# Performance work log

Measured on AMD Instinct MI355X. Metric: run time of the kernel, lower is better.

Reference implementation:

```python
import jax, jax.numpy as jnp
import numpy as np

NUM_HEADS = 8


def setup_inputs() -> dict:
    key = jax.random.key(0)
    ks = jax.random.split(key, 8)
    b, m, d = 8, 2048, 512
    sc = 1.0 / np.sqrt(d)
    return {
        "x": jax.random.normal(ks[0], (b, m, d), jnp.float32),
        "w_q": jax.random.normal(ks[1], (d, d), jnp.float32) * sc,
        "w_k": jax.random.normal(ks[2], (d, d), jnp.float32) * sc,
        "w_v": jax.random.normal(ks[3], (d, d), jnp.float32) * sc,
        "in_proj_w": jax.random.normal(ks[4], (3 * d, d), jnp.float32) * sc,
        "in_proj_b": jax.random.normal(ks[5], (3 * d,), jnp.float32) * 0.01,
        "out_w": jax.random.normal(ks[6], (d, d), jnp.float32) * sc,
        "out_b": jax.random.normal(ks[7], (d,), jnp.float32) * 0.01,
    }


def _rope_cos_sin(m, d):
    # faithful to source: theta = 10000 ** (-2*(i-1)/d), i = 0..d/2-1
    i = jnp.arange(d // 2, dtype=jnp.float32)
    theta = jnp.power(10000.0, -2.0 * (i - 1.0) / d)
    ang = jnp.arange(m, dtype=jnp.float32)[:, None] * theta  # [m, d/2]
    return jnp.cos(ang), jnp.sin(ang)


def reference(x, w_q, w_k, w_v, in_proj_w, in_proj_b, out_w, out_b):
    b, m, d = x.shape
    h, hd = NUM_HEADS, d // NUM_HEADS
    c, s = _rope_cos_sin(m, d)

    def rot(t):
        # equivalent to t[pos] @ R[pos] with the source's block-rotation matrix
        te = t.reshape(b, m, d // 2, 2)
        e, o = te[..., 0], te[..., 1]
        return jnp.stack([e * c + o * s, -e * s + o * c], axis=-1).reshape(b, m, d)

    q = rot(x @ w_q.T)
    k = rot(x @ w_k.T)
    v = rot(x @ w_v.T)

    # nn.MultiheadAttention's internal in_proj
    wqi, wki, wvi = jnp.split(in_proj_w, 3, axis=0)
    bqi, bki, bvi = jnp.split(in_proj_b, 3, axis=0)
    q = (q @ wqi.T + bqi).reshape(b, m, h, hd)
    k = (k @ wki.T + bki).reshape(b, m, h, hd)
    v = (v @ wvi.T + bvi).reshape(b, m, h, hd)

    scale = 1.0 / jnp.sqrt(jnp.asarray(hd, x.dtype))
    scores = jnp.einsum("bqhd,bkhd->bhqk", q, k) * scale
    causal = jnp.triu(jnp.ones((m, m), bool), k=1)
    scores = jnp.where(causal, jnp.finfo(x.dtype).min, scores)
    attn = jax.nn.softmax(scores, axis=-1)
    ctx = jnp.einsum("bhqk,bkhd->bqhd", attn, v).reshape(b, m, d)
    return ctx @ out_w.T + out_b
```

## Files before the change

### kernel.cpp

```cpp
#include <hip/hip_runtime.h>
#include <hip/hip_bf16.h>

typedef __attribute__((ext_vector_type(8))) short short8;
typedef __attribute__((ext_vector_type(4))) short short4v;
typedef __attribute__((ext_vector_type(4))) float f32x4;

__device__ __forceinline__ float bf2f(unsigned short u) {
    union { unsigned int i; float f; } v; v.i = ((unsigned int)u) << 16; return v.f;
}
__device__ __forceinline__ unsigned short f2bfh(float f) {
    union { __hip_bfloat16 h; unsigned short u; } c;
    c.h = __float2bfloat16(f);
    return c.u;
}

#define GLDS16(g, l) __builtin_amdgcn_global_load_lds( \
    (const __attribute__((address_space(1))) unsigned int*)(g), \
    (__attribute__((address_space(3))) unsigned int*)(l), 16, 0, 0)

__global__ __launch_bounds__(256) void cvt_one(
    const float* __restrict__ in, unsigned short* __restrict__ out, int nchunk)
{
    int i = blockIdx.x * 256 + threadIdx.x;
    if (i >= nchunk) return;
    f32x4 a = *(const f32x4*)&in[(size_t)i * 8];
    f32x4 b = *(const f32x4*)&in[(size_t)i * 8 + 4];
    short8 o;
    o[0] = (short)f2bfh(a[0]); o[1] = (short)f2bfh(a[1]);
    o[2] = (short)f2bfh(a[2]); o[3] = (short)f2bfh(a[3]);
    o[4] = (short)f2bfh(b[0]); o[5] = (short)f2bfh(b[1]);
    o[6] = (short)f2bfh(b[2]); o[7] = (short)f2bfh(b[3]);
    *(short8*)&out[(size_t)i * 8] = o;
}

__global__ __launch_bounds__(256) void cvt_w(
    const float* __restrict__ wq, const float* __restrict__ wk, const float* __restrict__ wv,
    const float* __restrict__ ipw, const float* __restrict__ ow,
    unsigned short* __restrict__ wqb, unsigned short* __restrict__ ipwb,
    unsigned short* __restrict__ owb)
{
    int z = blockIdx.y;
    const float* src;
    unsigned short* dst;
    if (z < 3)      { src = (z == 0 ? wq : z == 1 ? wk : wv); dst = wqb + (size_t)z * 262144; }
    else if (z < 6) { src = ipw + (size_t)(z - 3) * 262144;   dst = ipwb + (size_t)(z - 3) * 262144; }
    else            { src = ow;                                dst = owb; }
    int i = blockIdx.x * 256 + threadIdx.x;
    f32x4 a = *(const f32x4*)&src[(size_t)i * 8];
    f32x4 b = *(const f32x4*)&src[(size_t)i * 8 + 4];
    short8 o;
    o[0] = (short)f2bfh(a[0]); o[1] = (short)f2bfh(a[1]);
    o[2] = (short)f2bfh(a[2]); o[3] = (short)f2bfh(a[3]);
    o[4] = (short)f2bfh(b[0]); o[5] = (short)f2bfh(b[1]);
    o[6] = (short)f2bfh(b[2]); o[7] = (short)f2bfh(b[3]);
    *(short8*)&dst[(size_t)i * 8] = o;
}

__global__ __launch_bounds__(256) void rope_table(float* __restrict__ ct, float* __restrict__ st)
{
    int i = blockIdx.x;
    const float THC = -0.05190512648261308f;
    float theta = exp2f(THC * ((float)i - 1.0f));
    for (int k = 0; k < 8; ++k) {
        int pos = k * 256 + threadIdx.x;
        float sn, cs;
        sincosf((float)pos * theta, &sn, &cs);
        ct[i * 2048 + pos] = cs;
        st[i * 2048 + pos] = sn;
    }
}

__device__ __forceinline__ void gemm_core(
    const unsigned short* __restrict__ A, int lda,
    const unsigned short* __restrict__ B, int K,
    int rowBase, int colBase, int tid, int lane, int wave,
    short* As, short* Bs, f32x4 (&acc)[4][4])
{
    const int wr = wave >> 1, wc = wave & 1;
    const int lo = lane & 15, hi = lane >> 4;
    for (int k0 = 0; k0 < K; k0 += 64) {
        const unsigned short* Ab = A + (size_t)rowBase * lda + k0;
        const unsigned short* Bb = B + (size_t)colBase * K + k0;
        #pragma unroll
        for (int p = 0; p < 4; ++p) {
            int o = p * 256 + tid;
            GLDS16(&Ab[(size_t)(o >> 3) * lda + (o & 7) * 8], &As[o * 8]);
        }
        #pragma unroll
        for (int p = 0; p < 4; ++p) {
            int o = p * 256 + tid;
            GLDS16(&Bb[(size_t)(o >> 3) * K + (o & 7) * 8], &Bs[o * 8]);
        }
        __syncthreads();
        #pragma unroll
        for (int s = 0; s < 2; ++s) {
            short8 a[4], b[4];
            #pragma unroll
            for (int i = 0; i < 4; ++i)
                a[i] = *(const short8*)&As[(wr * 64 + i * 16 + lo) * 64 + s * 32 + hi * 8];
            #pragma unroll
            for (int j = 0; j < 4; ++j)
                b[j] = *(const short8*)&Bs[(wc * 64 + j * 16 + lo) * 64 + s * 32 + hi * 8];
            #pragma unroll
            for (int i = 0; i < 4; ++i)
                #pragma unroll
                for (int j = 0; j < 4; ++j)
                    acc[i][j] = __builtin_amdgcn_mfma_f32_16x16x32_bf16(a[i], b[j], acc[i][j], 0, 0, 0);
        }
        __syncthreads();
    }
}

template<int HAS_BIAS, int OUT>
__global__ __launch_bounds__(256) void gemm_bt(
    const unsigned short* __restrict__ A, int lda, const unsigned short* __restrict__ B,
    const float* __restrict__ bias, void* __restrict__ Cp,
    int M, int N, int K)
{
    __shared__ __align__(16) short As[128 * 64];
    __shared__ __align__(16) short Bs[128 * 64];
    const int tid = threadIdx.x, lane = tid & 63, wave = tid >> 6;
    const int wr = wave >> 1, wc = wave & 1;
    const int lo = lane & 15, hi = lane >> 4;
    const int rowBase = blockIdx.y * 128;
    const int colBase = blockIdx.x * 128;

    f32x4 acc[4][4] = {};
    gemm_core(A, lda, B, K, rowBase, colBase, tid, lane, wave, As, Bs, acc);

    #pragma unroll
    for (int i = 0; i < 4; ++i) {
        int rowA = rowBase + wr * 64 + i * 16 + hi * 4;
        #pragma unroll
        for (int j = 0; j < 4; ++j) {
            int col = colBase + wc * 64 + j * 16 + lo;
            float bv = HAS_BIAS ? bias[col] : 0.0f;
            #pragma unroll
            for (int r = 0; r < 4; ++r) {
                float v = acc[i][j][r] + bv;
                if (OUT == 1) ((float*)Cp)[(size_t)(rowA + r) * N + col] = v;
                else          ((unsigned short*)Cp)[(size_t)(rowA + r) * N + col] = f2bfh(v);
            }
        }
    }
}

__global__ __launch_bounds__(256) void gemm_rope(
    const unsigned short* __restrict__ A, const unsigned short* __restrict__ B,
    unsigned short* __restrict__ T,
    const float* __restrict__ ct, const float* __restrict__ st)
{
    __shared__ __align__(16) short As[128 * 64];
    __shared__ __align__(16) short Bs[128 * 64];
    const int tid = threadIdx.x, lane = tid & 63, wave = tid >> 6;
    const int wr = wave >> 1, wc = wave & 1;
    const int lo = lane & 15, hi = lane >> 4;
    const int rowBase = blockIdx.y * 128;
    const int colBase = blockIdx.x * 128;

    f32x4 acc[4][4] = {};
    gemm_core(A, 512, B, 512, rowBase, colBase, tid, lane, wave, As, Bs, acc);

    const float sgn = (lane & 1) ? -1.0f : 1.0f;
    #pragma unroll
    for (int i = 0; i < 4; ++i) {
        int rowA = rowBase + wr * 64 + i * 16 + hi * 4;
        int pos0 = rowA & 2047;
        #pragma unroll
        for (int j = 0; j < 4; ++j) {
            int col = colBase + wc * 64 + j * 16 + lo;
            int ii = (col & 511) >> 1;
            f32x4 cs = *(const f32x4*)&ct[ii * 2048 + pos0];
            f32x4 sn = *(const f32x4*)&st[ii * 2048 + pos0];
            #pragma unroll
            for (int r = 0; r < 4; ++r) {
                float v = acc[i][j][r];
                float p = __shfl_xor(v, 1);
                float o = v * cs[r] + sgn * p * sn[r];
                T[(size_t)(rowA + r) * 1536 + col] = f2bfh(o);
            }
        }
    }
}

__global__ __launch_bounds__(256) void gemm_inproj(
    const unsigned short* __restrict__ T, const unsigned short* __restrict__ ipwb,
    const float* __restrict__ ipb,
    unsigned short* __restrict__ Qb, unsigned short* __restrict__ Kb,
    unsigned short* __restrict__ Vt)
{
    __shared__ __align__(16) short As[128 * 64];
    __shared__ __align__(16) short Bs[128 * 64];
    const int tid = threadIdx.x, lane = tid & 63, wave = tid >> 6;
    const int wr = wave >> 1, wc = wave & 1;
    const int lo = lane & 15, hi = lane >> 4;
    const int rowBase = blockIdx.y * 128;
    const int colBase = blockIdx.x * 128;
    const int z = blockIdx.z;

    const unsigned short* A = T + z * 512;
    const unsigned short* B = ipwb + (size_t)z * 262144;
    const float* bias = ipb + z * 512;

    f32x4 acc[4][4] = {};
    gemm_core(A, 1536, B, 512, rowBase, colBase, tid, lane, wave, As, Bs, acc);

    unsigned short* Crm = (z == 0) ? Qb : Kb;
    #pragma unroll
    for (int i = 0; i < 4; ++i) {
        int rowA = rowBase + wr * 64 + i * 16 + hi * 4;
        #pragma unroll
        for (int j = 0; j < 4; ++j) {
            int col = colBase + wc * 64 + j * 16 + lo;
            float bv = bias[col];
            if (z == 2) {
                short4v sv;
                #pragma unroll
                for (int r = 0; r < 4; ++r) sv[r] = (short)f2bfh(acc[i][j][r] + bv);
                size_t idx = (((size_t)(rowA >> 11) * 8 + (col >> 6)) * 64 + (col & 63)) * 2048
                             + (rowA & 2047);
                *(short4v*)&Vt[idx] = sv;
            } else {
                #pragma unroll
                for (int r = 0; r < 4; ++r)
                    Crm[(size_t)(rowA + r) * 512 + col] = f2bfh(acc[i][j][r] + bv);
            }
        }
    }
}


__device__ __forceinline__ void attn_step(
    int kt, int NT, int qrow, int lo, int hi,
    const short* __restrict__ KsB, const short* __restrict__ VsB,
    short* __restrict__ Pw,
    short8 (&aq)[2], f32x4 (&o_acc)[4],
    float (&m_i)[4], float (&l_i)[4])
{
    const int swz = (lo & 7) << 3;

    f32x4 sa[4] = {};
    #pragma unroll
    for (int s = 0; s < 2; ++s) {
        short8 bk[4];
        #pragma unroll
        for (int n = 0; n < 4; ++n)
            bk[n] = *(const short8*)&KsB[(n * 16 + lo) * 64 + ((s * 32 + hi * 8) ^ swz)];
        #pragma unroll
        for (int n = 0; n < 4; ++n)
            sa[n] = __builtin_amdgcn_mfma_f32_16x16x32_bf16(aq[s], bk[n], sa[n], 0, 0, 0);
    }

    const bool need_mask = (kt == NT - 1);
    float sv[4][4];
    #pragma unroll
    for (int n = 0; n < 4; ++n) {
        int key = kt * 64 + n * 16 + lo;
        #pragma unroll
        for (int r = 0; r < 4; ++r) {
            float x = sa[n][r];
            if (need_mask) {
                int qr = qrow + hi * 4 + r;
                if (key > qr) x = -1e30f;
            }
            sv[n][r] = x;
        }
    }

    float alpha[4];
    #pragma unroll
    for (int r = 0; r < 4; ++r) {
        float x = fmaxf(fmaxf(sv[0][r], sv[1][r]), fmaxf(sv[2][r], sv[3][r]));
        #pragma unroll
        for (int off = 1; off < 16; off <<= 1) x = fmaxf(x, __shfl_xor(x, off));
        float mn = fmaxf(m_i[r], x);
        alpha[r] = __expf(m_i[r] - mn);
        m_i[r] = mn;
    }
    #pragma unroll
    for (int n = 0; n < 4; ++n)
        #pragma unroll
        for (int r = 0; r < 4; ++r)
            sv[n][r] = __expf(sv[n][r] - m_i[r]);

    #pragma unroll
    for (int r = 0; r < 4; ++r)
        l_i[r] = l_i[r] * alpha[r] + (sv[0][r] + sv[1][r]) + (sv[2][r] + sv[3][r]);

    #pragma unroll
    for (int t = 0; t < 4; ++t)
        #pragma unroll
        for (int r = 0; r < 4; ++r)
            o_acc[t][r] *= alpha[r];

    #pragma unroll
    for (int n = 0; n < 4; ++n)
        #pragma unroll
        for (int r = 0; r < 4; ++r) {
            int prow = hi * 4 + r;
            Pw[prow * 64 + ((n * 16 + lo) ^ ((prow & 7) << 3))] = (short)f2bfh(sv[n][r]);
        }

    #pragma unroll
    for (int s = 0; s < 2; ++s) {
        short8 ap = *(const short8*)&Pw[lo * 64 + ((s * 32 + hi * 8) ^ swz)];
        #pragma unroll
        for (int t = 0; t < 4; ++t) {
            short8 bv = *(const short8*)&VsB[(t * 16 + lo) * 64 + ((s * 32 + hi * 8) ^ swz)];
            o_acc[t] = __builtin_amdgcn_mfma_f32_16x16x32_bf16(ap, bv, o_acc[t], 0, 0, 0);
        }
    }
}

#define STG_LOAD(kt, KR0, KR1, VR0, VR1) { \
    int rr = tid >> 3, cc = (tid & 7) * 8; \
    KR0 = *(const short8*)&Kp[(rowQ + (size_t)((kt) * 64 + rr)) * 512 + colBase + cc]; \
    KR1 = *(const short8*)&Kp[(rowQ + (size_t)((kt) * 64 + rr + 32)) * 512 + colBase + cc]; \
    VR0 = *(const short8*)&Vh[(size_t)rr * 2048 + (kt) * 64 + cc]; \
    VR1 = *(const short8*)&Vh[(size_t)(rr + 32) * 2048 + (kt) * 64 + cc]; }

#define STG_WRITE(BUF, KR0, KR1, VR0, VR1) { \
    int rr = tid >> 3; \
    int sw = ((tid & 7) * 8) ^ ((rr & 7) << 3); \
    *(short8*)&Ks[BUF][rr * 64 + sw] = KR0; \
    *(short8*)&Ks[BUF][(rr + 32) * 64 + sw] = KR1; \
    *(short8*)&Vs[BUF][rr * 64 + sw] = VR0; \
    *(short8*)&Vs[BUF][(rr + 32) * 64 + sw] = VR1; }

__global__ __launch_bounds__(256, 3) void attn_kernel(
    const unsigned short* __restrict__ Q, const unsigned short* __restrict__ Kp,
    const unsigned short* __restrict__ Vt, unsigned short* __restrict__ O)
{
    const int tid = threadIdx.x, lane = tid & 63, wave = tid >> 6;
    const int lo = lane & 15, hi = lane >> 4;
    const int bh = blockIdx.x;
    const int qb = 31 - blockIdx.y;
    const int bb = bh >> 3, hh = bh & 7;
    const int NT = qb + 1;

    __shared__ __align__(16) short Ks[2][64 * 64];
    __shared__ __align__(16) short Vs[2][64 * 64];
    __shared__ __align__(16) short P[4][16 * 64];
    short* Pw = P[wave];

    const size_t rowQ = (size_t)bb * 2048;
    const int colBase = hh * 64;
    const unsigned short* Vh = Vt + (size_t)bh * 64 * 2048;
    const int qrow = qb * 64 + wave * 16;

    short8 aq[2];
    #pragma unroll
    for (int s = 0; s < 2; ++s) {
        aq[s] = *(const short8*)&Q[(rowQ + qrow + lo) * 512 + colBase + s * 32 + hi * 8];
        #pragma unroll
        for (int e = 0; e < 8; ++e)
            aq[s][e] = (short)f2bfh(bf2f((unsigned short)aq[s][e]) * 0.125f);
    }

    f32x4 o_acc[4] = {};
    float m_i[4], l_i[4];
    #pragma unroll
    for (int r = 0; r < 4; ++r) { m_i[r] = -1e30f; l_i[r] = 0.0f; }

    short8 ka0, ka1, va0, va1;
    short8 kb0, kb1, vb0, vb1;

    STG_LOAD(0, ka0, ka1, va0, va1);
    STG_WRITE(0, ka0, ka1, va0, va1);
    if (1 < NT) STG_LOAD(1, kb0, kb1, vb0, vb1);
    __syncthreads();

    for (int kt = 0; kt < NT; ) {
        if (kt + 1 < NT) STG_WRITE(1, kb0, kb1, vb0, vb1);
        if (kt + 2 < NT) STG_LOAD(kt + 2, ka0, ka1, va0, va1);
        attn_step(kt, NT, qrow, lo, hi, Ks[0], Vs[0], Pw, aq, o_acc, m_i, l_i);
        __syncthreads();
        ++kt;
        if (kt >= NT) break;
        if (kt + 1 < NT) STG_WRITE(0, ka0, ka1, va0, va1);
        if (kt + 2 < NT) STG_LOAD(kt + 2, kb0, kb1, vb0, vb1);
        attn_step(kt, NT, qrow, lo, hi, Ks[1], Vs[1], Pw, aq, o_acc, m_i, l_i);
        __syncthreads();
        ++kt;
    }

    #pragma unroll
    for (int r = 0; r < 4; ++r) {
        float x = l_i[r];
        #pragma unroll
        for (int off = 1; off < 16; off <<= 1) x += __shfl_xor(x, off);
        l_i[r] = x;
    }

    #pragma unroll
    for (int t = 0; t < 4; ++t)
        #pragma unroll
        for (int r = 0; r < 4; ++r) {
            float v = o_acc[t][r] / l_i[r];
            O[(rowQ + qrow + hi * 4 + r) * 512 + colBase + t * 16 + lo] = f2bfh(v);
        }
}

extern "C" void kernel_launch(void* const* d_in, const int* in_sizes, int n_in,
                              void* d_out, int out_size, void* d_ws, size_t ws_size,
                              hipStream_t stream)
{
    (void)in_sizes; (void)n_in; (void)out_size; (void)ws_size;
    const float* x   = (const float*)d_in[0];
    const float* w_q = (const float*)d_in[1];
    const float* w_k = (const float*)d_in[2];
    const float* w_v = (const float*)d_in[3];
    const float* ipw = (const float*)d_in[4];
    const float* ipb = (const float*)d_in[5];
    const float* ow  = (const float*)d_in[6];
    const float* ob  = (const float*)d_in[7];

    const int M = 16384;
    const size_t SZ = (size_t)M * 512;
    unsigned short* xb   = (unsigned short*)d_ws;
    unsigned short* wqb  = xb + SZ;
    unsigned short* ipwb = wqb + 786432;
    unsigned short* owb  = ipwb + 786432;
    unsigned short* T    = owb + 262144;
    unsigned short* Kb   = T + (size_t)M * 1536;
    unsigned short* Vt   = Kb + SZ;
    float* ct = (float*)(Vt + SZ);
    float* st = ct + 524288;
    unsigned short* Qb   = xb;
    unsigned short* Cb   = T;

    dim3 blk(256);

    cvt_one<<<dim3((int)(SZ / 8 / 256)), blk, 0, stream>>>(x, xb, (int)(SZ / 8));
    cvt_w<<<dim3(128, 7), blk, 0, stream>>>(w_q, w_k, w_v, ipw, ow, wqb, ipwb, owb);
    rope_table<<<dim3(256), blk, 0, stream>>>(ct, st);

    gemm_rope<<<dim3(12, 128), blk, 0, stream>>>(xb, wqb, T, ct, st);

    gemm_inproj<<<dim3(4, 128, 3), blk, 0, stream>>>(T, ipwb, ipb, Qb, Kb, Vt);

    attn_kernel<<<dim3(64, 32), blk, 0, stream>>>(Qb, Kb, Vt, Cb);

    gemm_bt<1, 1><<<dim3(4, 128), blk, 0, stream>>>(Cb, 512, owb, ob, (float*)d_out, M, 512, 512);
}
```

Before: 316.0 us.

## Compute transposed scores so P feeds PV MFMA from registers, dropping LDS round-trip

Swaps the operands of the QK^T MFMA so each lane holds a column of keys for one query row. The softmax row max and sum then need only two cross-lane shuffles instead of four. The probabilities are packed straight into 16x16x16 bf16 MFMA A-operands, which removes the per-wave P scratch in shared memory, its stores and reloads. The cost is twice as many, smaller PV MFMAs, extra shuffles to broadcast alpha and l to the output layout, and narrower V reads from LDS.

```diff
diff --git a/kernel.cpp b/kernel.cpp
--- a/kernel.cpp
+++ b/kernel.cpp
@@ -17,6 +17,12 @@
 #define GLDS16(g, l) __builtin_amdgcn_global_load_lds( \
     (const __attribute__((address_space(1))) unsigned int*)(g), \
     (__attribute__((address_space(3))) unsigned int*)(l), 16, 0, 0)
+
+#if __has_builtin(__builtin_amdgcn_mfma_f32_16x16x16_bf16)
+#define MFMA_PV(a, b, c) __builtin_amdgcn_mfma_f32_16x16x16_bf16(a, b, c, 0, 0, 0)
+#else
+#define MFMA_PV(a, b, c) __builtin_amdgcn_mfma_f32_16x16x16bf16_1k(a, b, c, 0, 0, 0)
+#endif
 
 __global__ __launch_bounds__(256) void cvt_one(
     const float* __restrict__ in, unsigned short* __restrict__ out, int nchunk)
@@ -233,9 +239,8 @@
 __device__ __forceinline__ void attn_step(
     int kt, int NT, int qrow, int lo, int hi,
     const short* __restrict__ KsB, const short* __restrict__ VsB,
-    short* __restrict__ Pw,
     short8 (&aq)[2], f32x4 (&o_acc)[4],
-    float (&m_i)[4], float (&l_i)[4])
+    float &m_i, float &l_i)
 {
     const int swz = (lo & 7) << 3;
 
@@ -248,68 +253,71 @@
             bk[n] = *(const short8*)&KsB[(n * 16 + lo) * 64 + ((s * 32 + hi * 8) ^ swz)];
         #pragma unroll
         for (int n = 0; n < 4; ++n)
-            sa[n] = __builtin_amdgcn_mfma_f32_16x16x32_bf16(aq[s], bk[n], sa[n], 0, 0, 0);
+            sa[n] = __builtin_amdgcn_mfma_f32_16x16x32_bf16(bk[n], aq[s], sa[n], 0, 0, 0);
     }
 
     const bool need_mask = (kt == NT - 1);
+    const int q = qrow + lo;
     float sv[4][4];
     #pragma unroll
-    for (int n = 0; n < 4; ++n) {
-        int key = kt * 64 + n * 16 + lo;
+    for (int n = 0; n < 4; ++n)
         #pragma unroll
         for (int r = 0; r < 4; ++r) {
             float x = sa[n][r];
             if (need_mask) {
-                int qr = qrow + hi * 4 + r;
-                if (key > qr) x = -1e30f;
+                int key = kt * 64 + n * 16 + hi * 4 + r;
+                if (key > q) x = -1e30f;
             }
             sv[n][r] = x;
         }
-    }
-
-    float alpha[4];
-    #pragma unroll
-    for (int r = 0; r < 4; ++r) {
-        float x = fmaxf(fmaxf(sv[0][r], sv[1][r]), fmaxf(sv[2][r], sv[3][r]));
-        #pragma unroll
-        for (int off = 1; off < 16; off <<= 1) x = fmaxf(x, __shfl_xor(x, off));
-        float mn = fmaxf(m_i[r], x);
-        alpha[r] = __expf(m_i[r] - mn);
-        m_i[r] = mn;
-    }
+
+    float mx0 = fmaxf(fmaxf(sv[0][0], sv[0][1]), fmaxf(sv[0][2], sv[0][3]));
+    float mx1 = fmaxf(fmaxf(sv[1][0], sv[1][1]), fmaxf(sv[1][2], sv[1][3]));
+    float mx2 = fmaxf(fmaxf(sv[2][0], sv[2][1]), fmaxf(sv[2][2], sv[2][3]));
+    float mx3 = fmaxf(fmaxf(sv[3][0], sv[3][1]), fmaxf(sv[3][2], sv[3][3]));
+    float mx = fmaxf(fmaxf(mx0, mx1), fmaxf(mx2, mx3));
+    mx = fmaxf(mx, __shfl_xor(mx, 16));
+    mx = fmaxf(mx, __shfl_xor(mx, 32));
+    float mn = fmaxf(m_i, mx);
+    float alpha = __expf(m_i - mn);
+    m_i = mn;
+
     #pragma unroll
     for (int n = 0; n < 4; ++n)
         #pragma unroll
         for (int r = 0; r < 4; ++r)
-            sv[n][r] = __expf(sv[n][r] - m_i[r]);
-
+            sv[n][r] = __expf(sv[n][r] - mn);
+
+    float s0 = (sv[0][0] + sv[0][1]) + (sv[0][2] + sv[0][3]);
+    float s1 = (sv[1][0] + sv[1][1]) + (sv[1][2] + sv[1][3]);
+    float s2 = (sv[2][0] + sv[2][1]) + (sv[2][2] + sv[2][3]);
+    float s3 = (sv[3][0] + sv[3][1]) + (sv[3][2] + sv[3][3]);
+    l_i = l_i * alpha + ((s0 + s1) + (s2 + s3));
+
+    float ar[4];
     #pragma unroll
     for (int r = 0; r < 4; ++r)
-        l_i[r] = l_i[r] * alpha[r] + (sv[0][r] + sv[1][r]) + (sv[2][r] + sv[3][r]);
-
+        ar[r] = __shfl(alpha, hi * 4 + r);
     #pragma unroll
     for (int t = 0; t < 4; ++t)
         #pragma unroll
         for (int r = 0; r < 4; ++r)
-            o_acc[t][r] *= alpha[r];
-
+            o_acc[t][r] *= ar[r];
+
+    short4v pa[4];
     #pragma unroll
     for (int n = 0; n < 4; ++n)
         #pragma unroll
-        for (int r = 0; r < 4; ++r) {
-            int prow = hi * 4 + r;
-            Pw[prow * 64 + ((n * 16 + lo) ^ ((prow & 7) << 3))] = (short)f2bfh(sv[n][r]);
-        }
-
-    #pragma unroll
-    for (int s = 0; s < 2; ++s) {
-        short8 ap = *(const short8*)&Pw[lo * 64 + ((s * 32 + hi * 8) ^ swz)];
+        for (int r = 0; r < 4; ++r)
+            pa[n][r] = (short)f2bfh(sv[n][r]);
+
+    #pragma unroll
+    for (int n = 0; n < 4; ++n)
         #pragma unroll
         for (int t = 0; t < 4; ++t) {
-            short8 bv = *(const short8*)&VsB[(t * 16 + lo) * 64 + ((s * 32 + hi * 8) ^ swz)];
-            o_acc[t] = __builtin_amdgcn_mfma_f32_16x16x32_bf16(ap, bv, o_acc[t], 0, 0, 0);
-        }
-    }
+            short4v vb = *(const short4v*)&VsB[(t * 16 + lo) * 64 + ((n * 16 + hi * 4) ^ swz)];
+            o_acc[t] = MFMA_PV(pa[n], vb, o_acc[t]);
+        }
 }
 
 #define STG_LOAD(kt, KR0, KR1, VR0, VR1) { \
@@ -340,8 +348,6 @@
 
     __shared__ __align__(16) short Ks[2][64 * 64];
     __shared__ __align__(16) short Vs[2][64 * 64];
-    __shared__ __align__(16) short P[4][16 * 64];
-    short* Pw = P[wave];
 
     const size_t rowQ = (size_t)bb * 2048;
     const int colBase = hh * 64;
@@ -358,9 +364,7 @@
     }
 
     f32x4 o_acc[4] = {};
-    float m_i[4], l_i[4];
-    #pragma unroll
-    for (int r = 0; r < 4; ++r) { m_i[r] = -1e30f; l_i[r] = 0.0f; }
+    float m_i = -1e30f, l_i = 0.0f;
 
     short8 ka0, ka1, va0, va1;
     short8 kb0, kb1, vb0, vb1;
@@ -373,30 +377,30 @@
     for (int kt = 0; kt < NT; ) {
         if (kt + 1 < NT) STG_WRITE(1, kb0, kb1, vb0, vb1);
         if (kt + 2 < NT) STG_LOAD(kt + 2, ka0, ka1, va0, va1);
-        attn_step(kt, NT, qrow, lo, hi, Ks[0], Vs[0], Pw, aq, o_acc, m_i, l_i);
+        attn_step(kt, NT, qrow, lo, hi, Ks[0], Vs[0], aq, o_acc, m_i, l_i);
         __syncthreads();
         ++kt;
         if (kt >= NT) break;
         if (kt + 1 < NT) STG_WRITE(0, ka0, ka1, va0, va1);
         if (kt + 2 < NT) STG_LOAD(kt + 2, kb0, kb1, vb0, vb1);
-        attn_step(kt, NT, qrow, lo, hi, Ks[1], Vs[1], Pw, aq, o_acc, m_i, l_i);
+        attn_step(kt, NT, qrow, lo, hi, Ks[1], Vs[1], aq, o_acc, m_i, l_i);
         __syncthreads();
         ++kt;
     }
 
-    #pragma unroll
-    for (int r = 0; r < 4; ++r) {
-        float x = l_i[r];
-        #pragma unroll
-        for (int off = 1; off < 16; off <<= 1) x += __shfl_xor(x, off);
-        l_i[r] = x;
-    }
+    float lt = l_i;
+    lt += __shfl_xor(lt, 16);
+    lt += __shfl_xor(lt, 32);
+    float lr[4];
+    #pragma unroll
+    for (int r = 0; r < 4; ++r)
+        lr[r] = __shfl(lt, hi * 4 + r);
 
     #pragma unroll
     for (int t = 0; t < 4; ++t)
         #pragma unroll
         for (int r = 0; r < 4; ++r) {
-            float v = o_acc[t][r] / l_i[r];
+            float v = o_acc[t][r] / lr[r];
             O[(rowQ + qrow + hi * 4 + r) * 512 + colBase + t * 16 + lo] = f2bfh(v);
         }
 }
```

New measurement: 304.1 us. -3.8%, faster.
